# Kernel tuning notes

Measured on AMD Instinct MI355X. Metric: run time of the kernel, lower is better.

## Reference

```python
import jax, jax.numpy as jnp
import numpy as np

N, E, F, H, OUT = 50000, 500000, 128, 128, 768

def _lin(x, W, b):
    return x @ W + b

def _layernorm(x, g, b, eps=1e-5):
    mu = jnp.mean(x, axis=-1, keepdims=True)
    var = jnp.var(x, axis=-1, keepdims=True)
    return (x - mu) * jax.lax.rsqrt(var + eps) * g + b

def _edge_softmax(alpha, dst, n_nodes):
    # softmax over incoming edges per destination node, per channel
    amax = jax.ops.segment_max(alpha, dst, num_segments=n_nodes)
    ex = jnp.exp(alpha - amax[dst])
    denom = jax.ops.segment_sum(ex, dst, num_segments=n_nodes)
    return ex / denom[dst]

def setup_inputs() -> dict:
    key = jax.random.key(0)
    ks = jax.random.split(key, 24)
    def w(k, i, o):
        return (jax.random.normal(k, (i, o), jnp.float32) / np.float32(np.sqrt(i)))
    inp = {
        'kind': jax.random.normal(ks[0], (N, F), jnp.float32),
        'edge_h': jax.random.normal(ks[1], (E, F), jnp.float32),
        'src': jax.random.randint(ks[2], (E,), 0, N, jnp.int32),
        'dst': jax.random.randint(ks[3], (E,), 0, N, jnp.int32),
        'KW': w(ks[4], 2 * F, H), 'Kb': jnp.zeros((H,), jnp.float32),
        'VW': w(ks[5], 2 * F, H), 'Vb': jnp.zeros((H,), jnp.float32),
        'QW': w(ks[6], F, H), 'Qb': jnp.zeros((H,), jnp.float32),
        'WW': w(ks[7], F + H, H), 'Wb': jnp.zeros((H,), jnp.float32),
        'K2W': w(ks[8], 3 * F, H), 'K2b': jnp.zeros((H,), jnp.float32),
        'V2W': w(ks[9], 3 * F, H), 'V2b': jnp.zeros((H,), jnp.float32),
        'Q2W': w(ks[10], 2 * F, H), 'Q2b': jnp.zeros((H,), jnp.float32),
        'W2W': w(ks[11], 2 * F + H, OUT), 'W2b': jnp.zeros((OUT,), jnp.float32),
        'ln1_g': jnp.ones((H,), jnp.float32), 'ln1_b': jnp.zeros((H,), jnp.float32),
        'ln2_g': jnp.ones((OUT,), jnp.float32), 'ln2_b': jnp.zeros((OUT,), jnp.float32),
        'gate_w': w(ks[12], OUT, 1), 'gate_b': jnp.zeros((1,), jnp.float32),
    }
    return inp

def reference(kind, edge_h, src, dst, KW, Kb, VW, Vb, QW, Qb, WW, Wb,
              K2W, K2b, V2W, V2b, Q2W, Q2b, W2W, W2b,
              ln1_g, ln1_b, ln2_g, ln2_b, gate_w, gate_b):
    n_nodes = kind.shape[0]
    src_kind = kind[src]                               # [E,F] gather
    # --- layer 1 ---
    Q = _lin(kind, QW, Qb)                             # [N,H]
    ek_in = jnp.concatenate([src_kind, edge_h], axis=1)  # [E,2F]
    eK = _lin(ek_in, KW, Kb)                           # [E,H]
    eV = _lin(ek_in, VW, Vb)                           # [E,H]
    alpha = _edge_softmax(Q[dst] * eK, dst, n_nodes)   # [E,H]
    h_n = jax.ops.segment_sum(alpha * eV, dst, num_segments=n_nodes)  # [N,H]
    h = _layernorm(_lin(jnp.concatenate([h_n, kind], axis=1), WW, Wb), ln1_g, ln1_b)
    # --- layer 2 ---
    Q2 = _lin(jnp.concatenate([kind, h], axis=1), Q2W, Q2b)            # [N,H]
    ek2_in = jnp.concatenate([src_kind, edge_h, h[src]], axis=1)       # [E,3F]
    eK2 = _lin(ek2_in, K2W, K2b)
    eV2 = _lin(ek2_in, V2W, V2b)
    alpha2 = _edge_softmax(Q2[dst] * eK2, dst, n_nodes)
    h_n1 = jax.ops.segment_sum(alpha2 * eV2, dst, num_segments=n_nodes)
    h1 = _layernorm(_lin(jnp.concatenate([h_n1, h, kind], axis=1), W2W, W2b), ln2_g, ln2_b)  # [N,768]
    # --- global attention pooling (single graph) ---
    gate = jax.nn.softmax(_lin(h1, gate_w, gate_b), axis=0)  # [N,1]
    graph_vec = jnp.sum(gate * h1, axis=0, keepdims=True)    # [1,768]
    return graph_vec
```

## Files before the change

kernel.cpp:

```cpp
#include <hip/hip_runtime.h>

typedef float f32x4 __attribute__((ext_vector_type(4)));
typedef short bf16x8 __attribute__((ext_vector_type(8)));
typedef unsigned short ushort8 __attribute__((ext_vector_type(8)));

__device__ __forceinline__ float bf2f(unsigned short u) {
    return __uint_as_float(((unsigned int)u) << 16);
}
__device__ __forceinline__ unsigned short f2bf(float f) {
    unsigned int u = __float_as_uint(f);
    u += 0x7FFFu + ((u >> 16) & 1u);
    return (unsigned short)(u >> 16);
}
__device__ __forceinline__ float pld(const void* p, long i, bool isbf) {
    return isbf ? bf2f(((const unsigned short*)p)[i]) : ((const float*)p)[i];
}

#define ASYNC16(gp, lp)                                                        \
    __builtin_amdgcn_global_load_lds(                                          \
        (__attribute__((address_space(1))) unsigned int*)(gp),                 \
        (__attribute__((address_space(3))) unsigned int*)(lp), 16, 0, 0)

__global__ void probe_kernel(const unsigned int* __restrict__ w, int* __restrict__ flag) {
    if (threadIdx.x == 0 && blockIdx.x == 0)
        *flag = (w[0] == 0x3F803F80u) ? 1 : 0;
}

__global__ __launch_bounds__(256) void cvt_kernel(
    const void* __restrict__ src_, unsigned short* __restrict__ dst_,
    const int* __restrict__ flag, long n8)
{
    const bool isbf = (*flag != 0);
    long stride = (long)gridDim.x * blockDim.x;
    for (long i = (long)blockIdx.x * blockDim.x + threadIdx.x; i < n8; i += stride) {
        if (isbf) {
            ((ushort8*)dst_)[i] = ((const ushort8*)src_)[i];
        } else {
            const float4* s = (const float4*)src_ + i * 2;
            float4 a = s[0], b = s[1];
            ushort8 r;
            r[0] = f2bf(a.x); r[1] = f2bf(a.y); r[2] = f2bf(a.z); r[3] = f2bf(a.w);
            r[4] = f2bf(b.x); r[5] = f2bf(b.y); r[6] = f2bf(b.z); r[7] = f2bf(b.w);
            ((ushort8*)dst_)[i] = r;
        }
    }
}

template <int WM, int WN>
__global__ __launch_bounds__(256) void gemm_kernel(
    const unsigned short* __restrict__ seg0, const unsigned short* __restrict__ seg1,
    const unsigned short* __restrict__ seg2,
    const int* __restrict__ gi0, const int* __restrict__ gi1, const int* __restrict__ gi2,
    const unsigned short* __restrict__ Bt, const float* __restrict__ bias,
    int M, int K, int Nout,
    float* __restrict__ outF, unsigned short* __restrict__ outB)
{
    constexpr int BM = WM * 64, BN = WN * 64;
    constexpr int AI = BM / 64;
    constexpr int BI = BN / 64;
    constexpr int PB = BN + 8;
    constexpr int STAGE = (BM + BN) * 32 * 2;
    constexpr int PANEL = 16 * PB * 4;
    constexpr int SH = STAGE > PANEL ? STAGE : PANEL;
    __shared__ __attribute__((aligned(16))) char shraw[SH];
    unsigned short* lA = (unsigned short*)shraw;
    unsigned short* lB = lA + BM * 32;

    const int tid  = threadIdx.x;
    const int wave = tid >> 6, lane = tid & 63;
    const int wm = wave / WN, wn = wave % WN;

    const int rsub = tid >> 2;
    const int csel = (tid & 3) ^ ((tid >> 3) & 3);

    const unsigned short* aptr0[AI];
    const unsigned short* aptr1[AI];
    const unsigned short* aptr2[AI];
#pragma unroll
    for (int i = 0; i < AI; ++i) {
        int gr = blockIdx.x * BM + rsub + 64 * i;
        if (gr >= M) gr = M - 1;
        aptr0[i] = seg0 + (long)(gi0 ? gi0[gr] : gr) * 128;
        aptr1[i] = seg1 ? seg1 + (long)(gi1 ? gi1[gr] : gr) * 128 : aptr0[i];
        aptr2[i] = seg2 ? seg2 + (long)(gi2 ? gi2[gr] : gr) * 128 : aptr0[i];
    }
    const unsigned short* bptr[BI];
#pragma unroll
    for (int i = 0; i < BI; ++i) {
        int bn = blockIdx.y * BN + rsub + 64 * i;
        bptr[i] = Bt + (long)bn * K;
    }

    f32x4 acc[4][4];
#pragma unroll
    for (int a = 0; a < 4; ++a)
#pragma unroll
        for (int b = 0; b < 4; ++b) acc[a][b] = (f32x4)(0.0f);

    const int q = lane >> 4, mrow = lane & 15;

    for (int kk = 0; kk < K; kk += 32) {
        __syncthreads();
        const int s = kk >> 7, koff = kk & 127;
#pragma unroll
        for (int i = 0; i < AI; ++i) {
            const unsigned short* ap = (s == 0) ? aptr0[i] : ((s == 1) ? aptr1[i] : aptr2[i]);
            ASYNC16(ap + koff + csel * 8, &lA[tid * 8 + i * 2048]);
        }
#pragma unroll
        for (int i = 0; i < BI; ++i) {
            ASYNC16(bptr[i] + kk + csel * 8, &lB[tid * 8 + i * 2048]);
        }
        __syncthreads();

        bf16x8 af[4], bfv[4];
#pragma unroll
        for (int t = 0; t < 4; ++t) {
            int r = wm * 64 + t * 16 + mrow;
            af[t] = *(const bf16x8*)&lA[r * 32 + ((q ^ ((r >> 1) & 3)) * 8)];
        }
#pragma unroll
        for (int t = 0; t < 4; ++t) {
            int r = wn * 64 + t * 16 + mrow;
            bfv[t] = *(const bf16x8*)&lB[r * 32 + ((q ^ ((r >> 1) & 3)) * 8)];
        }
#pragma unroll
        for (int tm = 0; tm < 4; ++tm)
#pragma unroll
            for (int tn = 0; tn < 4; ++tn)
                acc[tm][tn] = __builtin_amdgcn_mfma_f32_16x16x32_bf16(af[tm], bfv[tn], acc[tm][tn], 0, 0, 0);
    }

    float bv[4];
#pragma unroll
    for (int tn = 0; tn < 4; ++tn) {
        int col = blockIdx.y * BN + wn * 64 + tn * 16 + mrow;
        bv[tn] = bias ? bias[col] : 0.0f;
    }
    float*          pf = (float*)shraw;
    unsigned short* pb = (unsigned short*)shraw;

#pragma unroll
    for (int p = 0; p < BM / 16; ++p) {
        const int pw = p >> 2;
        const int tm = p & 3;
        __syncthreads();
        if (wm == pw) {
#pragma unroll
            for (int tn = 0; tn < 4; ++tn) {
                int cl = wn * 64 + tn * 16 + mrow;
#pragma unroll
                for (int r = 0; r < 4; ++r) {
                    int pr = q * 4 + r;
                    float v = acc[tm][tn][r] + bv[tn];
                    if (outF) pf[pr * PB + cl] = v;
                    else      pb[pr * PB + cl] = f2bf(v);
                }
            }
        }
        __syncthreads();
        const int rowbase = blockIdx.x * BM + p * 16;
        if (outF) {
            constexpr int CPR = BN / 4;
            for (int c = tid; c < 16 * CPR; c += 256) {
                int pr = c / CPR, co = (c - pr * CPR) * 4;
                int grow = rowbase + pr;
                if (grow < M)
                    *(float4*)(outF + (long)grow * Nout + blockIdx.y * BN + co) =
                        *(const float4*)(pf + pr * PB + co);
            }
        } else {
            constexpr int CPR = BN / 8;
            for (int c = tid; c < 16 * CPR; c += 256) {
                int pr = c / CPR, co = (c - pr * CPR) * 8;
                int grow = rowbase + pr;
                if (grow < M)
                    *(ushort8*)(outB + (long)grow * Nout + blockIdx.y * BN + co) =
                        *(const ushort8*)(pb + pr * PB + co);
            }
        }
    }
}

__global__ void hist_kernel(const int* __restrict__ dst, int* __restrict__ counts, int E) {
    int e = blockIdx.x * blockDim.x + threadIdx.x;
    if (e < E) atomicAdd(&counts[dst[e]], 1);
}

__global__ __launch_bounds__(1024) void scan_kernel(const int* __restrict__ counts,
                                                    int* __restrict__ indptr,
                                                    int* __restrict__ wp, int N) {
    __shared__ int wsum[16];
    __shared__ int carry;
    int tid = threadIdx.x;
    int wave = tid >> 6, lane = tid & 63;
    if (tid == 0) carry = 0;
    __syncthreads();
    for (int base = 0; base < N; base += 1024) {
        int c0 = carry;
        int i = base + tid;
        int v = (i < N) ? counts[i] : 0;
        int s = v;
#pragma unroll
        for (int off = 1; off < 64; off <<= 1) {
            int t = __shfl_up(s, off, 64);
            if (lane >= off) s += t;
        }
        if (lane == 63) wsum[wave] = s;
        __syncthreads();
        if (wave == 0 && lane < 16) {
            int w = wsum[lane];
#pragma unroll
            for (int off = 1; off < 16; off <<= 1) {
                int t = __shfl_up(w, off, 64);
                if (lane >= off) w += t;
            }
            wsum[lane] = w;
        }
        __syncthreads();
        int woff = wave ? wsum[wave - 1] : 0;
        if (i < N) { int ex = c0 + woff + s - v; indptr[i] = ex; wp[i] = ex; }
        __syncthreads();
        if (tid == 0) carry = c0 + wsum[15];
        __syncthreads();
    }
    if (tid == 0) indptr[N] = carry;
}

__global__ void scatter_kernel(const int* __restrict__ dst, int* __restrict__ wp,
                               int* __restrict__ eidx, int E) {
    int e = blockIdx.x * blockDim.x + threadIdx.x;
    if (e < E) {
        int slot = atomicAdd(&wp[dst[e]], 1);
        eidx[slot] = e;
    }
}

__global__ __launch_bounds__(256) void edge_softmax_kernel(
    const int* __restrict__ indptr, const int* __restrict__ eidx,
    const float* __restrict__ Q, const unsigned short* __restrict__ ekv,
    unsigned short* __restrict__ hn, int N)
{
    int wave = threadIdx.x >> 6, lane = threadIdx.x & 63;
    int n = blockIdx.x * 4 + wave;
    if (n >= N) return;
    int beg = indptr[n], end = indptr[n + 1];
    int c = lane << 1;
    float q0 = Q[(long)n * 128 + c], q1 = Q[(long)n * 128 + c + 1];
    float m0 = -3.4e38f, m1 = -3.4e38f, d0 = 0.f, d1 = 0.f, a0 = 0.f, a1 = 0.f;
    for (int i = beg; i < end; ++i) {
        int e = eidx[i];
        const unsigned short* er = ekv + (long)e * 256 + c;
        unsigned int kk = *(const unsigned int*)er;
        unsigned int vv = *(const unsigned int*)(er + 128);
        float k0 = bf2f((unsigned short)kk), k1 = bf2f((unsigned short)(kk >> 16));
        float v0 = bf2f((unsigned short)vv), v1 = bf2f((unsigned short)(vv >> 16));
        float s0 = q0 * k0, s1 = q1 * k1;
        float nm0 = fmaxf(m0, s0), nm1 = fmaxf(m1, s1);
        float e00 = __expf(m0 - nm0), e01 = __expf(s0 - nm0);
        float e10 = __expf(m1 - nm1), e11 = __expf(s1 - nm1);
        d0 = d0 * e00 + e01; a0 = a0 * e00 + e01 * v0; m0 = nm0;
        d1 = d1 * e10 + e11; a1 = a1 * e10 + e11 * v1; m1 = nm1;
    }
    float r0 = (end > beg) ? a0 / d0 : 0.f;
    float r1 = (end > beg) ? a1 / d1 : 0.f;
    unsigned int pk = (unsigned int)f2bf(r0) | ((unsigned int)f2bf(r1) << 16);
    *(unsigned int*)(hn + (long)n * 128 + c) = pk;
}

__global__ __launch_bounds__(256) void ln128_kernel(
    const float* __restrict__ x, const float* __restrict__ g,
    const float* __restrict__ b, unsigned short* __restrict__ y, int N)
{
    int wave = threadIdx.x >> 6, lane = threadIdx.x & 63;
    int n = blockIdx.x * 4 + wave;
    if (n >= N) return;
    int c = lane << 1;
    float2 v = *(const float2*)(x + (long)n * 128 + c);
    float s = v.x + v.y;
#pragma unroll
    for (int o = 1; o < 64; o <<= 1) s += __shfl_xor(s, o, 64);
    float mu = s * (1.f / 128.f);
    float dx0 = v.x - mu, dx1 = v.y - mu;
    float sq = dx0 * dx0 + dx1 * dx1;
#pragma unroll
    for (int o = 1; o < 64; o <<= 1) sq += __shfl_xor(sq, o, 64);
    float rs = rsqrtf(sq * (1.f / 128.f) + 1e-5f);
    float y0 = dx0 * rs * g[c] + b[c];
    float y1 = dx1 * rs * g[c + 1] + b[c + 1];
    unsigned int pk = (unsigned int)f2bf(y0) | ((unsigned int)f2bf(y1) << 16);
    *(unsigned int*)(y + (long)n * 128 + c) = pk;
}

__global__ __launch_bounds__(256) void ln768_kernel(
    const float* __restrict__ x, const float* __restrict__ g,
    const float* __restrict__ b, unsigned short* __restrict__ y, int N)
{
    __shared__ float red[4];
    int n = blockIdx.x;
    int tid = threadIdx.x;
    int wave = tid >> 6, lane = tid & 63;
    const float* xr = x + (long)n * 768;
    float v0 = xr[tid], v1 = xr[tid + 256], v2 = xr[tid + 512];
    float s = v0 + v1 + v2;
#pragma unroll
    for (int o = 1; o < 64; o <<= 1) s += __shfl_xor(s, o, 64);
    if (lane == 0) red[wave] = s;
    __syncthreads();
    float mu = (red[0] + red[1] + red[2] + red[3]) * (1.f / 768.f);
    float d0 = v0 - mu, d1 = v1 - mu, d2 = v2 - mu;
    float sq = d0 * d0 + d1 * d1 + d2 * d2;
#pragma unroll
    for (int o = 1; o < 64; o <<= 1) sq += __shfl_xor(sq, o, 64);
    __syncthreads();
    if (lane == 0) red[wave] = sq;
    __syncthreads();
    float rs = rsqrtf((red[0] + red[1] + red[2] + red[3]) * (1.f / 768.f) + 1e-5f);
    unsigned short* yr = y + (long)n * 768;
    yr[tid]       = f2bf(d0 * rs * g[tid]       + b[tid]);
    yr[tid + 256] = f2bf(d1 * rs * g[tid + 256] + b[tid + 256]);
    yr[tid + 512] = f2bf(d2 * rs * g[tid + 512] + b[tid + 512]);
}

__global__ __launch_bounds__(256) void gate_logits_kernel(
    const unsigned short* __restrict__ h1, const float* __restrict__ gw,
    const float* __restrict__ gb, float* __restrict__ gout, int N)
{
    int wave = threadIdx.x >> 6, lane = threadIdx.x & 63;
    int n = blockIdx.x * 4 + wave;
    if (n >= N) return;
    const unsigned short* hr = h1 + (long)n * 768;
    float s = 0.f;
#pragma unroll
    for (int t = 0; t < 3; ++t) {
        int c = lane * 4 + t * 256;
        unsigned int u0 = *(const unsigned int*)(hr + c);
        unsigned int u1 = *(const unsigned int*)(hr + c + 2);
        float4 w = *(const float4*)(gw + c);
        s += bf2f((unsigned short)u0) * w.x + bf2f((unsigned short)(u0 >> 16)) * w.y
           + bf2f((unsigned short)u1) * w.z + bf2f((unsigned short)(u1 >> 16)) * w.w;
    }
#pragma unroll
    for (int o = 1; o < 64; o <<= 1) s += __shfl_xor(s, o, 64);
    if (lane == 0) gout[n] = s + gb[0];
}

__global__ __launch_bounds__(256) void reduce_max_kernel(
    const float* __restrict__ gv, unsigned int* __restrict__ gmax, int N)
{
    __shared__ float red[4];
    int tid = threadIdx.x, wave = tid >> 6, lane = tid & 63;
    float m = -3.4e38f;
    for (int i = blockIdx.x * 256 + tid; i < N; i += gridDim.x * 256)
        m = fmaxf(m, gv[i]);
#pragma unroll
    for (int o = 1; o < 64; o <<= 1) m = fmaxf(m, __shfl_xor(m, o, 64));
    if (lane == 0) red[wave] = m;
    __syncthreads();
    if (tid == 0) {
        m = fmaxf(fmaxf(red[0], red[1]), fmaxf(red[2], red[3]));
        unsigned int u = __float_as_uint(m);
        u = (u & 0x80000000u) ? ~u : (u | 0x80000000u);
        atomicMax(gmax, u);
    }
}

__global__ __launch_bounds__(256) void gate_acc_kernel(
    const unsigned short* __restrict__ h1, const float* __restrict__ gv,
    const unsigned int* __restrict__ gmax_u, float* __restrict__ num,
    float* __restrict__ Z, int N)
{
    unsigned int mu = *gmax_u;
    float gm = (mu & 0x80000000u) ? __uint_as_float(mu & 0x7FFFFFFFu) : __uint_as_float(~mu);
    int tid = threadIdx.x;
    float a0 = 0.f, a1 = 0.f, a2 = 0.f, z = 0.f;
    for (int n = blockIdx.x; n < N; n += gridDim.x) {
        float ex = __expf(gv[n] - gm);
        const unsigned short* hr = h1 + (long)n * 768;
        a0 += ex * bf2f(hr[tid]);
        a1 += ex * bf2f(hr[tid + 256]);
        a2 += ex * bf2f(hr[tid + 512]);
        z += ex;
    }
    atomicAdd(num + tid, a0);
    atomicAdd(num + tid + 256, a1);
    atomicAdd(num + tid + 512, a2);
    if (tid == 0) atomicAdd(Z, z);
}

__global__ void finalize_kernel(const float* __restrict__ num, const float* __restrict__ Z,
                                void* __restrict__ out, const int* __restrict__ flag) {
    int i = blockIdx.x * blockDim.x + threadIdx.x;
    if (i < 768) {
        float v = num[i] / *Z;
        if (*flag) ((unsigned short*)out)[i] = f2bf(v);
        else       ((float*)out)[i] = v;
    }
}

__global__ void transpose_kernel(
    const void* QW, const void* KW, const void* VW, const void* WW,
    const void* Q2W, const void* K2W, const void* V2W, const void* W2W,
    unsigned short* tQ, unsigned short* tKV1, unsigned short* tW,
    unsigned short* tQ2, unsigned short* tKV2, unsigned short* tW2,
    const int* __restrict__ flag)
{
    const bool isbf = (*flag != 0);
    const void* srcp; unsigned short* dstp; int K, Nc;
    switch (blockIdx.y) {
        case 0: srcp = QW;  dstp = tQ;             K = 128; Nc = 128; break;
        case 1: srcp = KW;  dstp = tKV1;           K = 256; Nc = 128; break;
        case 2: srcp = VW;  dstp = tKV1 + 128*256; K = 256; Nc = 128; break;
        case 3: srcp = WW;  dstp = tW;             K = 256; Nc = 128; break;
        case 4: srcp = Q2W; dstp = tQ2;            K = 256; Nc = 128; break;
        case 5: srcp = K2W; dstp = tKV2;           K = 384; Nc = 128; break;
        case 6: srcp = V2W; dstp = tKV2 + 128*384; K = 384; Nc = 128; break;
        default: srcp = W2W; dstp = tW2;           K = 384; Nc = 768; break;
    }
    int total = K * Nc;
    for (int idx = blockIdx.x * blockDim.x + threadIdx.x; idx < total;
         idx += gridDim.x * blockDim.x) {
        int k = idx / Nc, nn = idx - k * Nc;
        dstp[nn * K + k] = f2bf(pld(srcp, idx, isbf));
    }
}

__global__ void init_kernel(
    const int* __restrict__ flag, int* counts, float* num, float* Z, unsigned int* gmax,
    const void* Qb, const void* Kb, const void* Vb, const void* Wb,
    const void* Q2b, const void* K2b, const void* V2b, const void* W2b,
    const void* l1g, const void* l1b, const void* l2g, const void* l2b,
    const void* gw, const void* gb,
    float* bQ, float* bKV, float* bW, float* bQ2, float* bKV2, float* bW2,
    float* f1g, float* f1b, float* f2g, float* f2b, float* fgw, float* fgb, int N)
{
    const bool isbf = (*flag != 0);
    int i = blockIdx.x * blockDim.x + threadIdx.x;
    if (i < N) counts[i] = 0;
    if (i < 768) {
        num[i] = 0.f;
        bW2[i] = pld(W2b, i, isbf);
        f2g[i] = pld(l2g, i, isbf); f2b[i] = pld(l2b, i, isbf);
        fgw[i] = pld(gw, i, isbf);
    }
    if (i < 128) {
        bQ[i] = pld(Qb, i, isbf); bW[i] = pld(Wb, i, isbf); bQ2[i] = pld(Q2b, i, isbf);
        bKV[i] = pld(Kb, i, isbf);  bKV[i + 128] = pld(Vb, i, isbf);
        bKV2[i] = pld(K2b, i, isbf); bKV2[i + 128] = pld(V2b, i, isbf);
        f1g[i] = pld(l1g, i, isbf); f1b[i] = pld(l1b, i, isbf);
    }
    if (i == 0) { *Z = 0.f; *gmax = 0u; fgb[0] = pld(gb, 0, isbf); }
}

extern "C" void kernel_launch(void* const* d_in, const int* in_sizes, int n_in,
                              void* d_out, int out_size, void* d_ws, size_t ws_size,
                              hipStream_t stream)
{
    const void* kind   = d_in[0];
    const void* edge_h = d_in[1];
    const int* src = (const int*)d_in[2];
    const int* dst = (const int*)d_in[3];
    const void* KW  = d_in[4];  const void* Kb  = d_in[5];
    const void* VW  = d_in[6];  const void* Vb  = d_in[7];
    const void* QW  = d_in[8];  const void* Qb  = d_in[9];
    const void* WW  = d_in[10]; const void* Wb  = d_in[11];
    const void* K2W = d_in[12]; const void* K2b = d_in[13];
    const void* V2W = d_in[14]; const void* V2b = d_in[15];
    const void* Q2W = d_in[16]; const void* Q2b = d_in[17];
    const void* W2W = d_in[18]; const void* W2b = d_in[19];
    const void* ln1g = d_in[20]; const void* ln1b = d_in[21];
    const void* ln2g = d_in[22]; const void* ln2b = d_in[23];
    const void* gw  = d_in[24]; const void* gb  = d_in[25];

    const int N = in_sizes[0] / 128;
    const int E = in_sizes[2];

    char* wsp = (char*)d_ws;
    auto alloc = [&](size_t bytes) -> char* {
        char* p = wsp;
        wsp += (bytes + 255) & ~(size_t)255;
        return p;
    };
    unsigned short* tQ   = (unsigned short*)alloc(128 * 128 * 2);
    unsigned short* tKV1 = (unsigned short*)alloc(256 * 256 * 2);
    unsigned short* tW   = (unsigned short*)alloc(128 * 256 * 2);
    unsigned short* tQ2  = (unsigned short*)alloc(128 * 256 * 2);
    unsigned short* tKV2 = (unsigned short*)alloc(256 * 384 * 2);
    unsigned short* tW2  = (unsigned short*)alloc(768 * 384 * 2);
    float* bQ   = (float*)alloc(128 * 4);
    float* bKV  = (float*)alloc(256 * 4);
    float* bW   = (float*)alloc(128 * 4);
    float* bQ2  = (float*)alloc(128 * 4);
    float* bKV2 = (float*)alloc(256 * 4);
    float* bW2  = (float*)alloc(768 * 4);
    float* f1g = (float*)alloc(128 * 4);
    float* f1b = (float*)alloc(128 * 4);
    float* f2g = (float*)alloc(768 * 4);
    float* f2b = (float*)alloc(768 * 4);
    float* fgw = (float*)alloc(768 * 4);
    float* fgb = (float*)alloc(256);
    int*   flag = (int*)alloc(256);
    unsigned short* kindB = (unsigned short*)alloc((size_t)N * 128 * 2);
    unsigned short* edgeB = (unsigned short*)alloc((size_t)E * 128 * 2);
    float* Qbuf = (float*)alloc((size_t)N * 128 * 4);

    size_t h1off = ((size_t)N * 768 * 4 + 255) & ~(size_t)255;
    size_t bigsz = (size_t)E * 512;
    size_t need  = h1off + (size_t)N * 768 * 2;
    if (need > bigsz) bigsz = need;
    char* big = alloc(bigsz);
    unsigned short* ekv   = (unsigned short*)big;
    float*          preh1 = (float*)big;
    unsigned short* h1    = (unsigned short*)(big + h1off);

    unsigned short* hn = (unsigned short*)alloc((size_t)N * 128 * 2);
    unsigned short* h  = (unsigned short*)alloc((size_t)N * 128 * 2);
    int* counts = (int*)alloc((size_t)N * 4);
    int* indptr = (int*)alloc((size_t)(N + 1) * 4);
    int* wp     = (int*)alloc((size_t)N * 4);
    int* eidx   = (int*)alloc((size_t)E * 4);
    float* g    = (float*)alloc((size_t)N * 4);
    unsigned int* gmaxp = (unsigned int*)alloc(256);
    float* Zp   = (float*)alloc(256);
    float* nump = (float*)alloc(768 * 4);

    probe_kernel<<<1, 64, 0, stream>>>((const unsigned int*)ln1g, flag);
    init_kernel<<<(N + 255) / 256, 256, 0, stream>>>(
        flag, counts, nump, Zp, gmaxp, Qb, Kb, Vb, Wb, Q2b, K2b, V2b, W2b,
        ln1g, ln1b, ln2g, ln2b, gw, gb,
        bQ, bKV, bW, bQ2, bKV2, bW2, f1g, f1b, f2g, f2b, fgw, fgb, N);
    transpose_kernel<<<dim3(64, 8), 256, 0, stream>>>(
        QW, KW, VW, WW, Q2W, K2W, V2W, W2W, tQ, tKV1, tW, tQ2, tKV2, tW2, flag);
    cvt_kernel<<<512, 256, 0, stream>>>(kind, kindB, flag, (long)N * 16);
    cvt_kernel<<<1024, 256, 0, stream>>>(edge_h, edgeB, flag, (long)E * 16);
    hist_kernel<<<(E + 255) / 256, 256, 0, stream>>>(dst, counts, E);
    scan_kernel<<<1, 1024, 0, stream>>>(counts, indptr, wp, N);
    scatter_kernel<<<(E + 255) / 256, 256, 0, stream>>>(dst, wp, eidx, E);

    gemm_kernel<2, 2><<<dim3((N + 127) / 128, 1), 256, 0, stream>>>(
        kindB, nullptr, nullptr, nullptr, nullptr, nullptr,
        tQ, bQ, N, 128, 128, Qbuf, nullptr);
    gemm_kernel<1, 4><<<dim3((E + 63) / 64, 1), 256, 0, stream>>>(
        kindB, edgeB, nullptr, src, nullptr, nullptr,
        tKV1, bKV, E, 256, 256, nullptr, ekv);
    edge_softmax_kernel<<<(N + 3) / 4, 256, 0, stream>>>(indptr, eidx, Qbuf, ekv, hn, N);
    gemm_kernel<2, 2><<<dim3((N + 127) / 128, 1), 256, 0, stream>>>(
        hn, kindB, nullptr, nullptr, nullptr, nullptr,
        tW, bW, N, 256, 128, Qbuf, nullptr);
    ln128_kernel<<<(N + 3) / 4, 256, 0, stream>>>(Qbuf, f1g, f1b, h, N);

    gemm_kernel<2, 2><<<dim3((N + 127) / 128, 1), 256, 0, stream>>>(
        kindB, h, nullptr, nullptr, nullptr, nullptr,
        tQ2, bQ2, N, 256, 128, Qbuf, nullptr);
    gemm_kernel<1, 4><<<dim3((E + 63) / 64, 1), 256, 0, stream>>>(
        kindB, edgeB, h, src, nullptr, src,
        tKV2, bKV2, E, 384, 256, nullptr, ekv);
    edge_softmax_kernel<<<(N + 3) / 4, 256, 0, stream>>>(indptr, eidx, Qbuf, ekv, hn, N);
    gemm_kernel<1, 4><<<dim3((N + 63) / 64, 3), 256, 0, stream>>>(
        hn, h, kindB, nullptr, nullptr, nullptr,
        tW2, bW2, N, 384, 768, preh1, nullptr);
    ln768_kernel<<<N, 256, 0, stream>>>(preh1, f2g, f2b, h1, N);

    gate_logits_kernel<<<(N + 3) / 4, 256, 0, stream>>>(h1, fgw, fgb, g, N);
    reduce_max_kernel<<<256, 256, 0, stream>>>(g, gmaxp, N);
    gate_acc_kernel<<<256, 256, 0, stream>>>(h1, g, gmaxp, nump, Zp, N);
    finalize_kernel<<<3, 256, 0, stream>>>(nump, Zp, d_out, flag);
}
```

Before: 1.382 ms.

## Split edge K/V projection into per-node and per-edge parts, fuse gate logits into LN

The K/V linear layers over concatenated [src_kind, edge_h, h[src]] inputs are split by linearity. The source-node parts are computed once per node (N rows) and gathered by src inside the edge softmax, so the per-edge GEMM only multiplies edge_h with K=128. This removes the redundant per-edge recomputation of node projections, at the cost of an extra gather per edge and a small bf16 rounding change from summing two separately rounded halves. The gate logit dot product is also fused into the 768-wide layernorm kernel, which removes one kernel launch and a reread of h1.

New measurement: 1.363 ms. About the same (-1.3%).

```diff
diff --git a/kernel.cpp b/kernel.cpp
--- a/kernel.cpp
+++ b/kernel.cpp
@@ -238,7 +238,9 @@
 
 __global__ __launch_bounds__(256) void edge_softmax_kernel(
     const int* __restrict__ indptr, const int* __restrict__ eidx,
+    const int* __restrict__ src,
     const float* __restrict__ Q, const unsigned short* __restrict__ ekv,
+    const unsigned short* __restrict__ nkv,
     unsigned short* __restrict__ hn, int N)
 {
     int wave = threadIdx.x >> 6, lane = threadIdx.x & 63;
@@ -250,11 +252,17 @@
     float m0 = -3.4e38f, m1 = -3.4e38f, d0 = 0.f, d1 = 0.f, a0 = 0.f, a1 = 0.f;
     for (int i = beg; i < end; ++i) {
         int e = eidx[i];
+        int sv = src[e];
         const unsigned short* er = ekv + (long)e * 256 + c;
+        const unsigned short* nr = nkv + (long)sv * 256 + c;
         unsigned int kk = *(const unsigned int*)er;
         unsigned int vv = *(const unsigned int*)(er + 128);
-        float k0 = bf2f((unsigned short)kk), k1 = bf2f((unsigned short)(kk >> 16));
-        float v0 = bf2f((unsigned short)vv), v1 = bf2f((unsigned short)(vv >> 16));
+        unsigned int nk = *(const unsigned int*)nr;
+        unsigned int nv = *(const unsigned int*)(nr + 128);
+        float k0 = bf2f((unsigned short)kk) + bf2f((unsigned short)nk);
+        float k1 = bf2f((unsigned short)(kk >> 16)) + bf2f((unsigned short)(nk >> 16));
+        float v0 = bf2f((unsigned short)vv) + bf2f((unsigned short)nv);
+        float v1 = bf2f((unsigned short)(vv >> 16)) + bf2f((unsigned short)(nv >> 16));
         float s0 = q0 * k0, s1 = q1 * k1;
         float nm0 = fmaxf(m0, s0), nm1 = fmaxf(m1, s1);
         float e00 = __expf(m0 - nm0), e01 = __expf(s0 - nm0);
@@ -294,9 +302,12 @@
 
 __global__ __launch_bounds__(256) void ln768_kernel(
     const float* __restrict__ x, const float* __restrict__ g,
-    const float* __restrict__ b, unsigned short* __restrict__ y, int N)
+    const float* __restrict__ b, const float* __restrict__ gw,
+    const float* __restrict__ gbias,
+    unsigned short* __restrict__ y, float* __restrict__ gout, int N)
 {
     __shared__ float red[4];
+    __shared__ float red2[4];
     int n = blockIdx.x;
     int tid = threadIdx.x;
     int wave = tid >> 6, lane = tid & 63;
@@ -316,33 +327,19 @@
     if (lane == 0) red[wave] = sq;
     __syncthreads();
     float rs = rsqrtf((red[0] + red[1] + red[2] + red[3]) * (1.f / 768.f) + 1e-5f);
+    float y0 = d0 * rs * g[tid]       + b[tid];
+    float y1 = d1 * rs * g[tid + 256] + b[tid + 256];
+    float y2 = d2 * rs * g[tid + 512] + b[tid + 512];
     unsigned short* yr = y + (long)n * 768;
-    yr[tid]       = f2bf(d0 * rs * g[tid]       + b[tid]);
-    yr[tid + 256] = f2bf(d1 * rs * g[tid + 256] + b[tid + 256]);
-    yr[tid + 512] = f2bf(d2 * rs * g[tid + 512] + b[tid + 512]);
-}
-
-__global__ __launch_bounds__(256) void gate_logits_kernel(
-    const unsigned short* __restrict__ h1, const float* __restrict__ gw,
-    const float* __restrict__ gb, float* __restrict__ gout, int N)
-{
-    int wave = threadIdx.x >> 6, lane = threadIdx.x & 63;
-    int n = blockIdx.x * 4 + wave;
-    if (n >= N) return;
-    const unsigned short* hr = h1 + (long)n * 768;
-    float s = 0.f;
-#pragma unroll
-    for (int t = 0; t < 3; ++t) {
-        int c = lane * 4 + t * 256;
-        unsigned int u0 = *(const unsigned int*)(hr + c);
-        unsigned int u1 = *(const unsigned int*)(hr + c + 2);
-        float4 w = *(const float4*)(gw + c);
-        s += bf2f((unsigned short)u0) * w.x + bf2f((unsigned short)(u0 >> 16)) * w.y
-           + bf2f((unsigned short)u1) * w.z + bf2f((unsigned short)(u1 >> 16)) * w.w;
-    }
-#pragma unroll
-    for (int o = 1; o < 64; o <<= 1) s += __shfl_xor(s, o, 64);
-    if (lane == 0) gout[n] = s + gb[0];
+    yr[tid]       = f2bf(y0);
+    yr[tid + 256] = f2bf(y1);
+    yr[tid + 512] = f2bf(y2);
+    float dot = y0 * gw[tid] + y1 * gw[tid + 256] + y2 * gw[tid + 512];
+#pragma unroll
+    for (int o = 1; o < 64; o <<= 1) dot += __shfl_xor(dot, o, 64);
+    if (lane == 0) red2[wave] = dot;
+    __syncthreads();
+    if (tid == 0) gout[n] = red2[0] + red2[1] + red2[2] + red2[3] + gbias[0];
 }
 
 __global__ __launch_bounds__(256) void reduce_max_kernel(
@@ -401,27 +398,41 @@
 __global__ void transpose_kernel(
     const void* QW, const void* KW, const void* VW, const void* WW,
     const void* Q2W, const void* K2W, const void* V2W, const void* W2W,
-    unsigned short* tQ, unsigned short* tKV1, unsigned short* tW,
-    unsigned short* tQ2, unsigned short* tKV2, unsigned short* tW2,
+    unsigned short* tQ, unsigned short* tNKV1, unsigned short* tEKV1,
+    unsigned short* tW, unsigned short* tQ2,
+    unsigned short* tNKV2, unsigned short* tEKV2, unsigned short* tW2,
     const int* __restrict__ flag)
 {
     const bool isbf = (*flag != 0);
-    const void* srcp; unsigned short* dstp; int K, Nc;
-    switch (blockIdx.y) {
-        case 0: srcp = QW;  dstp = tQ;             K = 128; Nc = 128; break;
-        case 1: srcp = KW;  dstp = tKV1;           K = 256; Nc = 128; break;
-        case 2: srcp = VW;  dstp = tKV1 + 128*256; K = 256; Nc = 128; break;
-        case 3: srcp = WW;  dstp = tW;             K = 256; Nc = 128; break;
-        case 4: srcp = Q2W; dstp = tQ2;            K = 256; Nc = 128; break;
-        case 5: srcp = K2W; dstp = tKV2;           K = 384; Nc = 128; break;
-        case 6: srcp = V2W; dstp = tKV2 + 128*384; K = 384; Nc = 128; break;
-        default: srcp = W2W; dstp = tW2;           K = 384; Nc = 768; break;
-    }
-    int total = K * Nc;
+    const int mode = blockIdx.y;
+    unsigned short* dstp; int Kd, Nr;
+    switch (mode) {
+        case 0:  dstp = tQ;    Kd = 128; Nr = 128; break;
+        case 1:  dstp = tNKV1; Kd = 128; Nr = 256; break;
+        case 2:  dstp = tEKV1; Kd = 128; Nr = 256; break;
+        case 3:  dstp = tW;    Kd = 256; Nr = 128; break;
+        case 4:  dstp = tQ2;   Kd = 256; Nr = 128; break;
+        case 5:  dstp = tNKV2; Kd = 256; Nr = 256; break;
+        case 6:  dstp = tEKV2; Kd = 128; Nr = 256; break;
+        default: dstp = tW2;   Kd = 384; Nr = 768; break;
+    }
+    int total = Kd * Nr;
     for (int idx = blockIdx.x * blockDim.x + threadIdx.x; idx < total;
          idx += gridDim.x * blockDim.x) {
-        int k = idx / Nc, nn = idx - k * Nc;
-        dstp[nn * K + k] = f2bf(pld(srcp, idx, isbf));
+        int n = idx / Kd, k = idx - n * Kd;
+        float v;
+        switch (mode) {
+            case 0:  v = pld(QW,  (long)k * 128 + n, isbf); break;
+            case 1:  v = pld(n < 128 ? KW : VW, (long)k * 128 + (n & 127), isbf); break;
+            case 2:  v = pld(n < 128 ? KW : VW, (long)(k + 128) * 128 + (n & 127), isbf); break;
+            case 3:  v = pld(WW,  (long)k * 128 + n, isbf); break;
+            case 4:  v = pld(Q2W, (long)k * 128 + n, isbf); break;
+            case 5:  v = pld(n < 128 ? K2W : V2W,
+                             (long)(k < 128 ? k : k + 128) * 128 + (n & 127), isbf); break;
+            case 6:  v = pld(n < 128 ? K2W : V2W, (long)(k + 128) * 128 + (n & 127), isbf); break;
+            default: v = pld(W2W, (long)k * 768 + n, isbf); break;
+        }
+        dstp[(long)n * Kd + k] = f2bf(v);
     }
 }
 
@@ -481,12 +492,14 @@
         wsp += (bytes + 255) & ~(size_t)255;
         return p;
     };
-    unsigned short* tQ   = (unsigned short*)alloc(128 * 128 * 2);
-    unsigned short* tKV1 = (unsigned short*)alloc(256 * 256 * 2);
-    unsigned short* tW   = (unsigned short*)alloc(128 * 256 * 2);
-    unsigned short* tQ2  = (unsigned short*)alloc(128 * 256 * 2);
-    unsigned short* tKV2 = (unsigned short*)alloc(256 * 384 * 2);
-    unsigned short* tW2  = (unsigned short*)alloc(768 * 384 * 2);
+    unsigned short* tQ    = (unsigned short*)alloc(128 * 128 * 2);
+    unsigned short* tNKV1 = (unsigned short*)alloc(256 * 128 * 2);
+    unsigned short* tEKV1 = (unsigned short*)alloc(256 * 128 * 2);
+    unsigned short* tW    = (unsigned short*)alloc(128 * 256 * 2);
+    unsigned short* tQ2   = (unsigned short*)alloc(128 * 256 * 2);
+    unsigned short* tNKV2 = (unsigned short*)alloc(256 * 256 * 2);
+    unsigned short* tEKV2 = (unsigned short*)alloc(256 * 128 * 2);
+    unsigned short* tW2   = (unsigned short*)alloc(768 * 384 * 2);
     float* bQ   = (float*)alloc(128 * 4);
     float* bKV  = (float*)alloc(256 * 4);
     float* bW   = (float*)alloc(128 * 4);
@@ -503,6 +516,8 @@
     unsigned short* kindB = (unsigned short*)alloc((size_t)N * 128 * 2);
     unsigned short* edgeB = (unsigned short*)alloc((size_t)E * 128 * 2);
     float* Qbuf = (float*)alloc((size_t)N * 128 * 4);
+    unsigned short* nkv1 = (unsigned short*)alloc((size_t)N * 256 * 2);
+    unsigned short* nkv2 = (unsigned short*)alloc((size_t)N * 256 * 2);
 
     size_t h1off = ((size_t)N * 768 * 4 + 255) & ~(size_t)255;
     size_t bigsz = (size_t)E * 512;
@@ -530,7 +545,8 @@
         ln1g, ln1b, ln2g, ln2b, gw, gb,
         bQ, bKV, bW, bQ2, bKV2, bW2, f1g, f1b, f2g, f2b, fgw, fgb, N);
     transpose_kernel<<<dim3(64, 8), 256, 0, stream>>>(
-        QW, KW, VW, WW, Q2W, K2W, V2W, W2W, tQ, tKV1, tW, tQ2, tKV2, tW2, flag);
+        QW, KW, VW, WW, Q2W, K2W, V2W, W2W,
+        tQ, tNKV1, tEKV1, tW, tQ2, tNKV2, tEKV2, tW2, flag);
     cvt_kernel<<<512, 256, 0, stream>>>(kind, kindB, flag, (long)N * 16);
     cvt_kernel<<<1024, 256, 0, stream>>>(edge_h, edgeB, flag, (long)E * 16);
     hist_kernel<<<(E + 255) / 256, 256, 0, stream>>>(dst, counts, E);
@@ -540,10 +556,14 @@
     gemm_kernel<2, 2><<<dim3((N + 127) / 128, 1), 256, 0, stream>>>(
         kindB, nullptr, nullptr, nullptr, nullptr, nullptr,
         tQ, bQ, N, 128, 128, Qbuf, nullptr);
+    gemm_kernel<2, 2><<<dim3((N + 127) / 128, 2), 256, 0, stream>>>(
+        kindB, nullptr, nullptr, nullptr, nullptr, nullptr,
+        tNKV1, bKV, N, 128, 256, nullptr, nkv1);
     gemm_kernel<1, 4><<<dim3((E + 63) / 64, 1), 256, 0, stream>>>(
-        kindB, edgeB, nullptr, src, nullptr, nullptr,
-        tKV1, bKV, E, 256, 256, nullptr, ekv);
-    edge_softmax_kernel<<<(N + 3) / 4, 256, 0, stream>>>(indptr, eidx, Qbuf, ekv, hn, N);
+        edgeB, nullptr, nullptr, nullptr, nullptr, nullptr,
+        tEKV1, nullptr, E, 128, 256, nullptr, ekv);
+    edge_softmax_kernel<<<(N + 3) / 4, 256, 0, stream>>>(
+        indptr, eidx, src, Qbuf, ekv, nkv1, hn, N);
     gemm_kernel<2, 2><<<dim3((N + 127) / 128, 1), 256, 0, stream>>>(
         hn, kindB, nullptr, nullptr, nullptr, nullptr,
         tW, bW, N, 256, 128, Qbuf, nullptr);
@@ -552,16 +572,19 @@
     gemm_kernel<2, 2><<<dim3((N + 127) / 128, 1), 256, 0, stream>>>(
         kindB, h, nullptr, nullptr, nullptr, nullptr,
         tQ2, bQ2, N, 256, 128, Qbuf, nullptr);
+    gemm_kernel<2, 2><<<dim3((N + 127) / 128, 2), 256, 0, stream>>>(
+        kindB, h, nullptr, nullptr, nullptr, nullptr,
+        tNKV2, bKV2, N, 256, 256, nullptr, nkv2);
     gemm_kernel<1, 4><<<dim3((E + 63) / 64, 1), 256, 0, stream>>>(
-        kindB, edgeB, h, src, nullptr, src,
-        tKV2, bKV2, E, 384, 256, nullptr, ekv);
-    edge_softmax_kernel<<<(N + 3) / 4, 256, 0, stream>>>(indptr, eidx, Qbuf, ekv, hn, N);
+        edgeB, nullptr, nullptr, nullptr, nullptr, nullptr,
+        tEKV2, nullptr, E, 128, 256, nullptr, ekv);
+    edge_softmax_kernel<<<(N + 3) / 4, 256, 0, stream>>>(
+        indptr, eidx, src, Qbuf, ekv, nkv2, hn, N);
     gemm_kernel<1, 4><<<dim3((N + 63) / 64, 3), 256, 0, stream>>>(
         hn, h, kindB, nullptr, nullptr, nullptr,
         tW2, bW2, N, 384, 768, preh1, nullptr);
-    ln768_kernel<<<N, 256, 0, stream>>>(preh1, f2g, f2b, h1, N);
-
-    gate_logits_kernel<<<(N + 3) / 4, 256, 0, stream>>>(h1, fgw, fgb, g, N);
+    ln768_kernel<<<N, 256, 0, stream>>>(preh1, f2g, f2b, fgw, fgb, h1, g, N);
+
     reduce_max_kernel<<<256, 256, 0, stream>>>(g, gmaxp, N);
     gate_acc_kernel<<<256, 256, 0, stream>>>(h1, g, gmaxp, nump, Zp, N);
     finalize_kernel<<<3, 256, 0, stream>>>(nump, Zp, d_out, flag);
```
